# Performance work log

Measured on AMD Instinct MI355X. Metric: run time of the kernel, lower is better.

Reference implementation:

```python
import jax, jax.numpy as jnp
import numpy as np

N_NODES = 50000
N_EDGES = 600000
F_NODE = 128
F_EDGE = 32
MSG = 32


def setup_inputs() -> dict:
    key = jax.random.key(0)
    k1, k2, k3, k4, k5, k6, k7 = jax.random.split(key, 7)
    node_features = jax.random.normal(k1, (N_NODES, F_NODE), dtype=jnp.float32)
    edge_node_indices = jax.random.randint(k2, (2, N_EDGES), 0, N_NODES, dtype=jnp.int64)
    edge_features = jax.random.normal(k3, (N_EDGES, F_EDGE), dtype=jnp.float32)
    edge_in = 2 * F_NODE + F_EDGE  # 288
    node_in = F_NODE + MSG  # 160
    s_e = 1.0 / np.sqrt(edge_in)
    s_n = 1.0 / np.sqrt(node_in)
    We = jax.random.uniform(k4, (edge_in, MSG), dtype=jnp.float32, minval=-s_e, maxval=s_e)
    be = jax.random.uniform(k5, (MSG,), dtype=jnp.float32, minval=-s_e, maxval=s_e)
    Wn = jax.random.uniform(k6, (node_in, F_NODE), dtype=jnp.float32, minval=-s_n, maxval=s_n)
    bn = jax.random.uniform(k7, (F_NODE,), dtype=jnp.float32, minval=-s_n, maxval=s_n)
    return {
        "node_features": node_features,
        "edge_node_indices": edge_node_indices,
        "edge_features": edge_features,
        "We": We, "be": be, "Wn": Wn, "bn": bn,
    }


def reference(node_features, edge_node_indices, edge_features, We, be, Wn, bn):
    node0, node1 = edge_node_indices[0], edge_node_indices[1]
    # gather endpoint features per edge: [E, 2*Fn + Fe]
    msg_in = jnp.concatenate(
        [node_features[node0], node_features[node1], edge_features], axis=1
    )
    messages = jax.nn.relu(msg_in @ We + be)  # [E, MSG]
    # scatter-sum messages into source nodes (scatter index = node0)
    msg_sums = jax.ops.segment_sum(messages, node0, num_segments=node_features.shape[0])
    node_in = jnp.concatenate([node_features, msg_sums], axis=1)  # [N, Fn+MSG]
    return jax.nn.relu(node_in @ Wn + bn)  # [N, Fn]
```

## Files before the change

### kernel.cpp

```cpp
#include <hip/hip_runtime.h>

#define N_NODES 50000
#define N_EDGES 600000
#define F_NODE 128
#define F_EDGE 32
#define MSG 32
#define NPB 32
#define CHK 128
#define QB64 ((N_NODES + 63) / 64)
#define FBLOCKS ((N_NODES + NPB - 1) / NPB)
#define CBLOCKS ((N_EDGES + 255) / 256)

typedef float v2f __attribute__((ext_vector_type(2)));

__device__ __forceinline__ unsigned short f2bf(float f) {
    union { float f; unsigned int u; } v; v.f = f;
    unsigned int r = v.u + 0x7fffu + ((v.u >> 16) & 1u);
    return (unsigned short)(r >> 16);
}

#define BAR_LGKM() do {                                           \
    asm volatile("s_waitcnt lgkmcnt(0)" ::: "memory");            \
    __builtin_amdgcn_s_barrier();                                 \
    asm volatile("" ::: "memory");                                \
} while (0)

__global__ __launch_bounds__(256)
void hist_kernel(const float* __restrict__ nf,
                 const float* __restrict__ We,
                 const float* __restrict__ be,
                 const int* __restrict__ idx,
                 unsigned short* __restrict__ Q,
                 unsigned short* __restrict__ P0g,
                 int* __restrict__ deg,
                 int* __restrict__ rank)
{
    if (blockIdx.x >= QB64) {
        int e = (blockIdx.x - QB64) * 256 + threadIdx.x;
        if (e < N_EDGES) {
            int n = idx[e];
            if ((unsigned)n >= (unsigned)N_NODES) n = 0;
            rank[e] = atomicAdd(&deg[n], 1);
        }
        return;
    }
    __shared__ float sInT[32 * 64];
    __shared__ float sWeA[32 * 32];
    __shared__ float sWeB[32 * 32];

    const int tid = threadIdx.x;
    const int n0b = blockIdx.x * 64;
    const int ng = tid & 31;
    const int og = tid >> 5;

    v2f accA[4], accB[4];
#pragma unroll
    for (int j = 0; j < 4; ++j) { accA[j] = (v2f){0.f, 0.f}; accB[j] = (v2f){0.f, 0.f}; }

    for (int kc = 0; kc < 4; ++kc) {
        __syncthreads();
        ((float4*)sWeA)[tid] = ((const float4*)(We + kc * 32 * MSG))[tid];
        ((float4*)sWeB)[tid] = ((const float4*)(We + (128 + kc * 32) * MSG))[tid];
        {
            int nl = tid >> 2, q = tid & 3;
            int n = n0b + nl; if (n >= N_NODES) n = N_NODES - 1;
            const float4* src4 = (const float4*)(nf + (size_t)n * F_NODE + kc * 32);
#pragma unroll
            for (int h = 0; h < 2; ++h) {
                float4 v = src4[q * 2 + h];
                int kl = q * 8 + h * 4;
                sInT[(kl + 0) * 64 + nl] = v.x;
                sInT[(kl + 1) * 64 + nl] = v.y;
                sInT[(kl + 2) * 64 + nl] = v.z;
                sInT[(kl + 3) * 64 + nl] = v.w;
            }
        }
        __syncthreads();
#pragma unroll
        for (int k = 0; k < 32; ++k) {
            v2f m = *(const v2f*)&sInT[k * 64 + 2 * ng];
            float4 wa = *(const float4*)&sWeA[k * 32 + og * 4];
            float4 wb = *(const float4*)&sWeB[k * 32 + og * 4];
            accA[0] += m * wa.x; accA[1] += m * wa.y;
            accA[2] += m * wa.z; accA[3] += m * wa.w;
            accB[0] += m * wb.x; accB[1] += m * wb.y;
            accB[2] += m * wb.z; accB[3] += m * wb.w;
        }
    }
    float bloc[4];
#pragma unroll
    for (int j = 0; j < 4; ++j) bloc[j] = be[og * 4 + j];
#pragma unroll
    for (int i = 0; i < 2; ++i) {
        int n = n0b + 2 * ng + i;
        if (n < N_NODES) {
            ushort4 oq, op;
            oq.x = f2bf(accB[0][i]); oq.y = f2bf(accB[1][i]);
            oq.z = f2bf(accB[2][i]); oq.w = f2bf(accB[3][i]);
            op.x = f2bf(accA[0][i] + bloc[0]); op.y = f2bf(accA[1][i] + bloc[1]);
            op.z = f2bf(accA[2][i] + bloc[2]); op.w = f2bf(accA[3][i] + bloc[3]);
            *(ushort4*)(Q   + (size_t)n * MSG + og * 4) = oq;
            *(ushort4*)(P0g + (size_t)n * MSG + og * 4) = op;
        }
    }
}

__global__ __launch_bounds__(1024)
void scan_kernel(int* __restrict__ deg_cursor) {
    __shared__ int wsum[16];
    __shared__ int wpre[16];
    const int t = threadIdx.x;
    const int lane = t & 63;
    const int wid = t >> 6;
    const int N4 = N_NODES / 4;
    const int NT = (N4 + 1023) / 1024;
    int run = 0;
    int4 vnext = make_int4(0, 0, 0, 0);
    if (t < N4) vnext = ((const int4*)deg_cursor)[t];
    for (int tt = 0; tt < NT; ++tt) {
        int4 v = vnext;
        if (tt + 1 < NT) {
            int ni = (tt + 1) * 1024 + t;
            vnext = (ni < N4) ? ((const int4*)deg_cursor)[ni] : make_int4(0, 0, 0, 0);
        }
        int s = v.x + v.y + v.z + v.w;
        int x = s;
#pragma unroll
        for (int d = 1; d < 64; d <<= 1) {
            int u = __shfl_up(x, (unsigned)d, 64);
            if (lane >= d) x += u;
        }
        if (lane == 63) wsum[wid] = x;
        BAR_LGKM();
        if (wid == 0) {
            int ss = (lane < 16) ? wsum[lane] : 0;
#pragma unroll
            for (int d = 1; d < 16; d <<= 1) {
                int u = __shfl_up(ss, (unsigned)d, 64);
                if (lane >= d) ss += u;
            }
            if (lane < 16) wpre[lane] = ss;
        }
        BAR_LGKM();
        int wexcl = (wid > 0) ? wpre[wid - 1] : 0;
        int total = wpre[15];
        int i4 = tt * 1024 + t;
        if (i4 < N4) {
            int base = run + wexcl + (x - s);
            int4 o;
            o.x = base;
            o.y = base + v.x;
            o.z = base + v.x + v.y;
            o.w = base + v.x + v.y + v.z;
            ((int4*)deg_cursor)[i4] = o;
        }
        run += total;
        BAR_LGKM();
    }
}

__global__ void place_kernel(const int* __restrict__ idx,
                             const int* __restrict__ startArr,
                             const int* __restrict__ rank,
                             int* __restrict__ perm) {
    int e = blockIdx.x * 256 + threadIdx.x;
    if (e < N_EDGES) {
        int n = idx[e];
        if ((unsigned)n >= (unsigned)N_NODES) n = 0;
        int p = startArr[n] + rank[e];
        if ((unsigned)p < (unsigned)N_EDGES) perm[p] = e;
    }
}

__global__ __launch_bounds__(256, 4)
void fused_kernel(const float* __restrict__ nf,
                  const int* __restrict__ idx,
                  const float* __restrict__ ef,
                  const float* __restrict__ We,
                  const float* __restrict__ Wn,
                  const float* __restrict__ bn,
                  const int* __restrict__ perm,
                  const int* __restrict__ startArr,
                  const unsigned short* __restrict__ Q,
                  const unsigned short* __restrict__ P0g,
                  float* __restrict__ out)
{
    __shared__ __align__(16) float S[9892];
    float* sBuf = S;
    float* sMsg = S + 4096;
    float* sWeC = S + 8192;
    unsigned short* sP0h = (unsigned short*)(S + 9216);
    int* sNL  = (int*)(S + 9728);
    int* sOff = (int*)(S + 9856);
    float* sWn   = S;
    float* sInT2 = S + 4096;

    const int tid = threadIdx.x;
    const int n0b = blockIdx.x * NPB;

    if (tid <= NPB) {
        int nn = n0b + tid;
        int v = (nn < N_NODES) ? startArr[nn] : N_EDGES;
        if (v < 0) v = 0;
        if (v > N_EDGES) v = N_EDGES;
        sOff[tid] = v;
    }
    ((float4*)sWeC)[tid] = ((const float4*)(We + 256 * MSG))[tid];
    if (tid < 128) {
        int r = tid >> 2, c = (tid & 3) * 8;
        int n = n0b + r; if (n >= N_NODES) n = N_NODES - 1;
        *(uint4*)(sP0h + r * MSG + c) = *(const uint4*)(P0g + (size_t)n * MSG + c);
    }
    __syncthreads();

    const int rs = sOff[0];
    const int re = sOff[NPB];

    float msum[4];
#pragma unroll
    for (int j = 0; j < 4; ++j) msum[j] = 0.f;
    const int rnl = tid >> 3;
    const int rq4 = (tid & 7) * 4;
    const int gx  = (rq4 >> 3) << 2;

    const int eq = tid & 31;
    const int cq = tid >> 5;
    const int g1 = (cq >> 1) & 3;
    const int el = tid >> 1;
    const int h2 = tid & 1;

    int n1r = 0;
    int pe_next = 0, pe_next2 = 0;
    float4 efr[4];
#pragma unroll
    for (int q = 0; q < 4; ++q) efr[q] = make_float4(0.f, 0.f, 0.f, 0.f);

    if (rs < re) {
        int e0 = rs + el;
        int pe0 = 0;
        if (e0 < re) {
            pe0 = perm[e0];
            if ((unsigned)pe0 >= (unsigned)N_EDGES) pe0 = 0;
            if (h2 == 0) {
                int tn = idx[N_EDGES + pe0];
                if ((unsigned)tn >= (unsigned)N_NODES) tn = 0;
                n1r = tn;
            }
        }
        const float4* ef4 = (const float4*)(ef + (size_t)pe0 * F_EDGE + h2 * 16);
#pragma unroll
        for (int q = 0; q < 4; ++q) efr[q] = ef4[q];
        int e1 = rs + CHK + el;
        if (e1 < re) {
            int p = perm[e1];
            if ((unsigned)p >= (unsigned)N_EDGES) p = 0;
            pe_next = p;
        }
        pe_next2 = pe_next;
    }

    for (int cs = rs; cs < re; cs += CHK) {
        pe_next = pe_next2;
        {
#pragma unroll
            for (int q = 0; q < 4; ++q) {
                float4 v = efr[q];
                int g = (h2 * 2 + (q >> 1)) & 3;
                int ctw = ((el & ~3) ^ (g << 2)) + (el & 3);
                int r0 = (h2 * 16 + q * 4) * CHK;
                sBuf[r0 + 0 * CHK + ctw] = v.x;
                sBuf[r0 + 1 * CHK + ctw] = v.y;
                sBuf[r0 + 2 * CHK + ctw] = v.z;
                sBuf[r0 + 3 * CHK + ctw] = v.w;
            }
            if (h2 == 0) {
                int e = cs + el;
                int ln = 0;
                if (e < re) {
                    int lo = 0, hi = NPB;
#pragma unroll
                    for (int s = 0; s < 5; ++s) {
                        int mid = (lo + hi) >> 1;
                        if (sOff[mid] <= e) lo = mid; else hi = mid;
                    }
                    ln = lo;
                }
                sNL[el] = (ln << 20) | n1r;
            }
            int e1 = cs + CHK + el;
            if (e1 < re) {
                int pe1 = pe_next;
                if (h2 == 0) {
                    int tn = idx[N_EDGES + pe1];
                    if ((unsigned)tn >= (unsigned)N_NODES) tn = 0;
                    n1r = tn;
                }
                const float4* ef4 = (const float4*)(ef + (size_t)pe1 * F_EDGE + h2 * 16);
#pragma unroll
                for (int q = 0; q < 4; ++q) efr[q] = ef4[q];
            } else if (h2 == 0) n1r = 0;
            int e2 = cs + 2 * CHK + el;
            if (e2 < re) {
                int p = perm[e2];
                if ((unsigned)p >= (unsigned)N_EDGES) p = 0;
                pe_next2 = p;
            } else pe_next2 = 0;
        }
        BAR_LGKM();

        int4 nlq = *(const int4*)&sNL[4 * eq];
        int nlv[4] = { nlq.x, nlq.y, nlq.z, nlq.w };
        uint2 qv[4];
#pragma unroll
        for (int i = 0; i < 4; ++i)
            qv[i] = *(const uint2*)(Q + (size_t)(nlv[i] & 0xFFFFF) * MSG + cq * 4);

        v2f accp[4][2];
#pragma unroll
        for (int j = 0; j < 4; ++j) { accp[j][0] = (v2f){0.f,0.f}; accp[j][1] = (v2f){0.f,0.f}; }

#pragma unroll
        for (int k = 0; k < 32; ++k) {
            float4 m4 = *(const float4*)&sBuf[k * CHK + ((4 * eq) ^ (((k >> 3) & 3) << 2))];
            float4 w  = *(const float4*)&sWeC[k * 32 + cq * 4];
            v2f m01 = (v2f){m4.x, m4.y}, m23 = (v2f){m4.z, m4.w};
            accp[0][0] += m01 * w.x; accp[0][1] += m23 * w.x;
            accp[1][0] += m01 * w.y; accp[1][1] += m23 * w.y;
            accp[2][0] += m01 * w.z; accp[2][1] += m23 * w.z;
            accp[3][0] += m01 * w.w; accp[3][1] += m23 * w.w;
        }

        {
            uint2 pv[4];
#pragma unroll
            for (int i = 0; i < 4; ++i)
                pv[i] = *(const uint2*)(sP0h + (nlv[i] >> 20) * MSG + cq * 4);
            int sb = (4 * eq) ^ (g1 << 2);
#pragma unroll
            for (int j = 0; j < 4; ++j) {
                float sv[4];
#pragma unroll
                for (int i = 0; i < 4; ++i) {
                    unsigned qu = (j < 2) ? qv[i].x : qv[i].y;
                    unsigned pu = (j < 2) ? pv[i].x : pv[i].y;
                    float qf = __uint_as_float((j & 1) ? (qu & 0xffff0000u) : (qu << 16));
                    float pf = __uint_as_float((j & 1) ? (pu & 0xffff0000u) : (pu << 16));
                    sv[i] = fmaxf(accp[j][i >> 1][i & 1] + pf + qf, 0.f);
                }
                *(float4*)&sMsg[(cq * 4 + j) * CHK + sb] =
                    make_float4(sv[0], sv[1], sv[2], sv[3]);
            }
        }
        BAR_LGKM();

        {
            int lo = sOff[rnl] - cs;     if (lo < 0) lo = 0;
            int hi = sOff[rnl + 1] - cs; if (hi > CHK) hi = CHK;
            for (int elr = lo; elr < hi; ++elr) {
                int ebase = ((elr & ~3) ^ gx) + (elr & 3);
#pragma unroll
                for (int j = 0; j < 4; ++j)
                    msum[j] += sMsg[(rq4 + j) * CHK + ebase];
            }
        }
    }

    const int png = tid & 7;
    const int pcg = tid >> 3;

    v2f acc2[4][2];
#pragma unroll
    for (int j = 0; j < 4; ++j) { acc2[j][0] = (v2f){0.f,0.f}; acc2[j][1] = (v2f){0.f,0.f}; }

    for (int kc = 0; kc < 5; ++kc) {
        __syncthreads();
        {
            const float4* w4 = (const float4*)(Wn + (size_t)kc * 32 * 128);
            float4* s4 = (float4*)sWn;
#pragma unroll
            for (int i = 0; i < 4; ++i) s4[tid + 256 * i] = w4[tid + 256 * i];
        }
        {
            if (kc < 4) {
                int nl = tid >> 3, q = tid & 7;
                int n = n0b + nl; if (n >= N_NODES) n = N_NODES - 1;
                float4 v = *(const float4*)(nf + (size_t)n * F_NODE + kc * 32 + q * 4);
#pragma unroll
                for (int h = 0; h < 4; ++h) {
                    int r = q * 4 + h;
                    sInT2[r * 32 + (nl ^ ((r & 7) << 2))] = (&v.x)[h];
                }
            } else {
#pragma unroll
                for (int h = 0; h < 4; ++h) {
                    int r = rq4 + h;
                    sInT2[r * 32 + (rnl ^ ((r & 7) << 2))] = msum[h];
                }
            }
        }
        __syncthreads();

#pragma unroll
        for (int k = 0; k < 32; ++k) {
            float4 m4 = *(const float4*)&sInT2[k * 32 + ((4 * png) ^ ((k & 7) << 2))];
            float4 w  = *(const float4*)&sWn[k * 128 + 4 * pcg];
            v2f m01 = (v2f){m4.x, m4.y}, m23 = (v2f){m4.z, m4.w};
            acc2[0][0] += m01 * w.x; acc2[0][1] += m23 * w.x;
            acc2[1][0] += m01 * w.y; acc2[1][1] += m23 * w.y;
            acc2[2][0] += m01 * w.z; acc2[2][1] += m23 * w.z;
            acc2[3][0] += m01 * w.w; acc2[3][1] += m23 * w.w;
        }
    }

    {
        float4 bnv = *(const float4*)(bn + 4 * pcg);
#pragma unroll
        for (int p = 0; p < 2; ++p)
#pragma unroll
            for (int l = 0; l < 2; ++l) {
                int n = n0b + 4 * png + 2 * p + l;
                if (n < N_NODES) {
                    float4 v;
                    v.x = fmaxf(acc2[0][p][l] + bnv.x, 0.f);
                    v.y = fmaxf(acc2[1][p][l] + bnv.y, 0.f);
                    v.z = fmaxf(acc2[2][p][l] + bnv.z, 0.f);
                    v.w = fmaxf(acc2[3][p][l] + bnv.w, 0.f);
                    *(float4*)(out + (size_t)n * F_NODE + 4 * pcg) = v;
                }
            }
    }
}

extern "C" void kernel_launch(void* const* d_in, const int* in_sizes, int n_in,
                              void* d_out, int out_size, void* d_ws, size_t ws_size,
                              hipStream_t stream) {
    const float* nf  = (const float*)d_in[0];
    const int*   idx = (const int*)d_in[1];
    const float* ef  = (const float*)d_in[2];
    const float* We  = (const float*)d_in[3];
    const float* be  = (const float*)d_in[4];
    const float* Wn  = (const float*)d_in[5];
    const float* bn  = (const float*)d_in[6];
    float* out = (float*)d_out;

    int* deg  = (int*)d_ws;
    int* rank = deg + N_NODES;
    int* perm = rank + N_EDGES;
    unsigned short* Q   = (unsigned short*)(perm + N_EDGES);
    unsigned short* P0g = Q + (size_t)N_NODES * MSG;

    hipMemsetAsync(deg, 0, (size_t)N_NODES * sizeof(int), stream);

    hist_kernel<<<QB64 + CBLOCKS, 256, 0, stream>>>(nf, We, be, idx, Q, P0g, deg, rank);
    scan_kernel<<<1, 1024, 0, stream>>>(deg);
    place_kernel<<<CBLOCKS, 256, 0, stream>>>(idx, deg, rank, perm);

    fused_kernel<<<FBLOCKS, 256, 0, stream>>>(
        nf, idx, ef, We, Wn, bn, perm, deg, Q, P0g, out);
}
```

Baseline: 260.3 us.

## Precompute node-feature half of node MLP in histogram kernel as bf16

Moves the node_features@Wn[0:128] + bn part of the node update out of the fused kernel and into extra blocks of the histogram kernel. Those blocks write the partial product to a bf16 workspace buffer, so the fused kernel only does the message-sum chunk (K=32) and adds the stored partial. This is meant to shorten the fused kernel's tail and overlap the dense GEMM with the edge histogram work. In exchange it adds a 50000x128 bf16 write and read, and rounding the partial to bf16 reduces accuracy.

After: 655.3 us. 152% more time.

```diff
diff --git a/kernel.cpp b/kernel.cpp
--- a/kernel.cpp
+++ b/kernel.cpp
@@ -29,14 +29,20 @@
 void hist_kernel(const float* __restrict__ nf,
                  const float* __restrict__ We,
                  const float* __restrict__ be,
+                 const float* __restrict__ Wn,
+                 const float* __restrict__ bn,
                  const int* __restrict__ idx,
                  unsigned short* __restrict__ Q,
                  unsigned short* __restrict__ P0g,
+                 unsigned short* __restrict__ OP,
                  int* __restrict__ deg,
                  int* __restrict__ rank)
 {
-    if (blockIdx.x >= QB64) {
-        int e = (blockIdx.x - QB64) * 256 + threadIdx.x;
+    __shared__ __align__(16) float S[6144];
+    const int tid = threadIdx.x;
+
+    if (blockIdx.x >= 2 * QB64) {
+        int e = (blockIdx.x - 2 * QB64) * 256 + tid;
         if (e < N_EDGES) {
             int n = idx[e];
             if ((unsigned)n >= (unsigned)N_NODES) n = 0;
@@ -44,63 +50,138 @@
         }
         return;
     }
-    __shared__ float sInT[32 * 64];
-    __shared__ float sWeA[32 * 32];
-    __shared__ float sWeB[32 * 32];
-
-    const int tid = threadIdx.x;
-    const int n0b = blockIdx.x * 64;
-    const int ng = tid & 31;
-    const int og = tid >> 5;
-
-    v2f accA[4], accB[4];
-#pragma unroll
-    for (int j = 0; j < 4; ++j) { accA[j] = (v2f){0.f, 0.f}; accB[j] = (v2f){0.f, 0.f}; }
-
-    for (int kc = 0; kc < 4; ++kc) {
-        __syncthreads();
-        ((float4*)sWeA)[tid] = ((const float4*)(We + kc * 32 * MSG))[tid];
-        ((float4*)sWeB)[tid] = ((const float4*)(We + (128 + kc * 32) * MSG))[tid];
-        {
-            int nl = tid >> 2, q = tid & 3;
-            int n = n0b + nl; if (n >= N_NODES) n = N_NODES - 1;
-            const float4* src4 = (const float4*)(nf + (size_t)n * F_NODE + kc * 32);
-#pragma unroll
-            for (int h = 0; h < 2; ++h) {
-                float4 v = src4[q * 2 + h];
-                int kl = q * 8 + h * 4;
-                sInT[(kl + 0) * 64 + nl] = v.x;
-                sInT[(kl + 1) * 64 + nl] = v.y;
-                sInT[(kl + 2) * 64 + nl] = v.z;
-                sInT[(kl + 3) * 64 + nl] = v.w;
-            }
-        }
-        __syncthreads();
-#pragma unroll
-        for (int k = 0; k < 32; ++k) {
-            v2f m = *(const v2f*)&sInT[k * 64 + 2 * ng];
-            float4 wa = *(const float4*)&sWeA[k * 32 + og * 4];
-            float4 wb = *(const float4*)&sWeB[k * 32 + og * 4];
-            accA[0] += m * wa.x; accA[1] += m * wa.y;
-            accA[2] += m * wa.z; accA[3] += m * wa.w;
-            accB[0] += m * wb.x; accB[1] += m * wb.y;
-            accB[2] += m * wb.z; accB[3] += m * wb.w;
-        }
-    }
-    float bloc[4];
-#pragma unroll
-    for (int j = 0; j < 4; ++j) bloc[j] = be[og * 4 + j];
-#pragma unroll
-    for (int i = 0; i < 2; ++i) {
-        int n = n0b + 2 * ng + i;
-        if (n < N_NODES) {
-            ushort4 oq, op;
-            oq.x = f2bf(accB[0][i]); oq.y = f2bf(accB[1][i]);
-            oq.z = f2bf(accB[2][i]); oq.w = f2bf(accB[3][i]);
-            op.x = f2bf(accA[0][i] + bloc[0]); op.y = f2bf(accA[1][i] + bloc[1]);
-            op.z = f2bf(accA[2][i] + bloc[2]); op.w = f2bf(accA[3][i] + bloc[3]);
-            *(ushort4*)(Q   + (size_t)n * MSG + og * 4) = oq;
-            *(ushort4*)(P0g + (size_t)n * MSG + og * 4) = op;
+
+    if (blockIdx.x >= QB64) {
+        float* sInT = S;
+        float* sWn  = S + 2048;
+        const int n0b = (blockIdx.x - QB64) * 64;
+        const int png2 = tid >> 4;
+        const int pcg2 = tid & 15;
+
+        v2f accC[8][2];
+#pragma unroll
+        for (int j = 0; j < 8; ++j) { accC[j][0] = (v2f){0.f,0.f}; accC[j][1] = (v2f){0.f,0.f}; }
+
+        for (int kc = 0; kc < 4; ++kc) {
+            __syncthreads();
+            {
+                const float4* w4 = (const float4*)(Wn + (size_t)kc * 32 * 128);
+                float4* s4 = (float4*)sWn;
+#pragma unroll
+                for (int i = 0; i < 4; ++i) s4[tid + 256 * i] = w4[tid + 256 * i];
+            }
+            {
+                int nl = tid >> 2, q = tid & 3;
+                int n = n0b + nl; if (n >= N_NODES) n = N_NODES - 1;
+                const float4* src4 = (const float4*)(nf + (size_t)n * F_NODE + kc * 32);
+#pragma unroll
+                for (int h = 0; h < 2; ++h) {
+                    float4 v = src4[q * 2 + h];
+                    int kl = q * 8 + h * 4;
+                    sInT[(kl + 0) * 64 + nl] = v.x;
+                    sInT[(kl + 1) * 64 + nl] = v.y;
+                    sInT[(kl + 2) * 64 + nl] = v.z;
+                    sInT[(kl + 3) * 64 + nl] = v.w;
+                }
+            }
+            __syncthreads();
+#pragma unroll
+            for (int k = 0; k < 32; ++k) {
+                float4 m4 = *(const float4*)&sInT[k * 64 + 4 * png2];
+                float4 w0 = *(const float4*)&sWn[k * 128 + 4 * pcg2];
+                float4 w1 = *(const float4*)&sWn[k * 128 + 64 + 4 * pcg2];
+                v2f m01 = (v2f){m4.x, m4.y}, m23 = (v2f){m4.z, m4.w};
+                accC[0][0] += m01 * w0.x; accC[0][1] += m23 * w0.x;
+                accC[1][0] += m01 * w0.y; accC[1][1] += m23 * w0.y;
+                accC[2][0] += m01 * w0.z; accC[2][1] += m23 * w0.z;
+                accC[3][0] += m01 * w0.w; accC[3][1] += m23 * w0.w;
+                accC[4][0] += m01 * w1.x; accC[4][1] += m23 * w1.x;
+                accC[5][0] += m01 * w1.y; accC[5][1] += m23 * w1.y;
+                accC[6][0] += m01 * w1.z; accC[6][1] += m23 * w1.z;
+                accC[7][0] += m01 * w1.w; accC[7][1] += m23 * w1.w;
+            }
+        }
+        float4 b0 = *(const float4*)(bn + 4 * pcg2);
+        float4 b1 = *(const float4*)(bn + 64 + 4 * pcg2);
+#pragma unroll
+        for (int p = 0; p < 2; ++p)
+#pragma unroll
+            for (int l = 0; l < 2; ++l) {
+                int n = n0b + 4 * png2 + 2 * p + l;
+                if (n < N_NODES) {
+                    ushort4 o0, o1;
+                    o0.x = f2bf(accC[0][p][l] + b0.x);
+                    o0.y = f2bf(accC[1][p][l] + b0.y);
+                    o0.z = f2bf(accC[2][p][l] + b0.z);
+                    o0.w = f2bf(accC[3][p][l] + b0.w);
+                    o1.x = f2bf(accC[4][p][l] + b1.x);
+                    o1.y = f2bf(accC[5][p][l] + b1.y);
+                    o1.z = f2bf(accC[6][p][l] + b1.z);
+                    o1.w = f2bf(accC[7][p][l] + b1.w);
+                    *(ushort4*)(OP + (size_t)n * F_NODE + 4 * pcg2) = o0;
+                    *(ushort4*)(OP + (size_t)n * F_NODE + 64 + 4 * pcg2) = o1;
+                }
+            }
+        return;
+    }
+
+    {
+        float* sInT = S;
+        float* sWeA = S + 2048;
+        float* sWeB = S + 3072;
+        const int n0b = blockIdx.x * 64;
+        const int ng = tid & 31;
+        const int og = tid >> 5;
+
+        v2f accA[4], accB[4];
+#pragma unroll
+        for (int j = 0; j < 4; ++j) { accA[j] = (v2f){0.f, 0.f}; accB[j] = (v2f){0.f, 0.f}; }
+
+        for (int kc = 0; kc < 4; ++kc) {
+            __syncthreads();
+            ((float4*)sWeA)[tid] = ((const float4*)(We + kc * 32 * MSG))[tid];
+            ((float4*)sWeB)[tid] = ((const float4*)(We + (128 + kc * 32) * MSG))[tid];
+            {
+                int nl = tid >> 2, q = tid & 3;
+                int n = n0b + nl; if (n >= N_NODES) n = N_NODES - 1;
+                const float4* src4 = (const float4*)(nf + (size_t)n * F_NODE + kc * 32);
+#pragma unroll
+                for (int h = 0; h < 2; ++h) {
+                    float4 v = src4[q * 2 + h];
+                    int kl = q * 8 + h * 4;
+                    sInT[(kl + 0) * 64 + nl] = v.x;
+                    sInT[(kl + 1) * 64 + nl] = v.y;
+                    sInT[(kl + 2) * 64 + nl] = v.z;
+                    sInT[(kl + 3) * 64 + nl] = v.w;
+                }
+            }
+            __syncthreads();
+#pragma unroll
+            for (int k = 0; k < 32; ++k) {
+                v2f m = *(const v2f*)&sInT[k * 64 + 2 * ng];
+                float4 wa = *(const float4*)&sWeA[k * 32 + og * 4];
+                float4 wb = *(const float4*)&sWeB[k * 32 + og * 4];
+                accA[0] += m * wa.x; accA[1] += m * wa.y;
+                accA[2] += m * wa.z; accA[3] += m * wa.w;
+                accB[0] += m * wb.x; accB[1] += m * wb.y;
+                accB[2] += m * wb.z; accB[3] += m * wb.w;
+            }
+        }
+        float bloc[4];
+#pragma unroll
+        for (int j = 0; j < 4; ++j) bloc[j] = be[og * 4 + j];
+#pragma unroll
+        for (int i = 0; i < 2; ++i) {
+            int n = n0b + 2 * ng + i;
+            if (n < N_NODES) {
+                ushort4 oq, op;
+                oq.x = f2bf(accB[0][i]); oq.y = f2bf(accB[1][i]);
+                oq.z = f2bf(accB[2][i]); oq.w = f2bf(accB[3][i]);
+                op.x = f2bf(accA[0][i] + bloc[0]); op.y = f2bf(accA[1][i] + bloc[1]);
+                op.z = f2bf(accA[2][i] + bloc[2]); op.w = f2bf(accA[3][i] + bloc[3]);
+                *(ushort4*)(Q   + (size_t)n * MSG + og * 4) = oq;
+                *(ushort4*)(P0g + (size_t)n * MSG + og * 4) = op;
+            }
         }
     }
 }
@@ -178,11 +259,11 @@
                   const float* __restrict__ ef,
                   const float* __restrict__ We,
                   const float* __restrict__ Wn,
-                  const float* __restrict__ bn,
                   const int* __restrict__ perm,
                   const int* __restrict__ startArr,
                   const unsigned short* __restrict__ Q,
                   const unsigned short* __restrict__ P0g,
+                  const unsigned short* __restrict__ OP,
                   float* __restrict__ out)
 {
     __shared__ __align__(16) float S[9892];
@@ -192,7 +273,7 @@
     unsigned short* sP0h = (unsigned short*)(S + 9216);
     int* sNL  = (int*)(S + 9728);
     int* sOff = (int*)(S + 9856);
-    float* sWn   = S;
+    float* sWn2  = S;
     float* sInT2 = S + 4096;
 
     const int tid = threadIdx.x;
@@ -368,63 +449,48 @@
     const int png = tid & 7;
     const int pcg = tid >> 3;
 
+    __syncthreads();
+    {
+        const float4* w4 = (const float4*)(Wn + (size_t)128 * 128);
+        float4* s4 = (float4*)sWn2;
+#pragma unroll
+        for (int i = 0; i < 4; ++i) s4[tid + 256 * i] = w4[tid + 256 * i];
+#pragma unroll
+        for (int h = 0; h < 4; ++h) {
+            int r = rq4 + h;
+            sInT2[r * 32 + (rnl ^ ((r & 7) << 2))] = msum[h];
+        }
+    }
+    __syncthreads();
+
     v2f acc2[4][2];
 #pragma unroll
     for (int j = 0; j < 4; ++j) { acc2[j][0] = (v2f){0.f,0.f}; acc2[j][1] = (v2f){0.f,0.f}; }
 
-    for (int kc = 0; kc < 5; ++kc) {
-        __syncthreads();
-        {
-            const float4* w4 = (const float4*)(Wn + (size_t)kc * 32 * 128);
-            float4* s4 = (float4*)sWn;
-#pragma unroll
-            for (int i = 0; i < 4; ++i) s4[tid + 256 * i] = w4[tid + 256 * i];
-        }
-        {
-            if (kc < 4) {
-                int nl = tid >> 3, q = tid & 7;
-                int n = n0b + nl; if (n >= N_NODES) n = N_NODES - 1;
-                float4 v = *(const float4*)(nf + (size_t)n * F_NODE + kc * 32 + q * 4);
-#pragma unroll
-                for (int h = 0; h < 4; ++h) {
-                    int r = q * 4 + h;
-                    sInT2[r * 32 + (nl ^ ((r & 7) << 2))] = (&v.x)[h];
-                }
-            } else {
-#pragma unroll
-                for (int h = 0; h < 4; ++h) {
-                    int r = rq4 + h;
-                    sInT2[r * 32 + (rnl ^ ((r & 7) << 2))] = msum[h];
-                }
-            }
-        }
-        __syncthreads();
-
-#pragma unroll
-        for (int k = 0; k < 32; ++k) {
-            float4 m4 = *(const float4*)&sInT2[k * 32 + ((4 * png) ^ ((k & 7) << 2))];
-            float4 w  = *(const float4*)&sWn[k * 128 + 4 * pcg];
-            v2f m01 = (v2f){m4.x, m4.y}, m23 = (v2f){m4.z, m4.w};
-            acc2[0][0] += m01 * w.x; acc2[0][1] += m23 * w.x;
-            acc2[1][0] += m01 * w.y; acc2[1][1] += m23 * w.y;
-            acc2[2][0] += m01 * w.z; acc2[2][1] += m23 * w.z;
-            acc2[3][0] += m01 * w.w; acc2[3][1] += m23 * w.w;
-        }
+#pragma unroll
+    for (int k = 0; k < 32; ++k) {
+        float4 m4 = *(const float4*)&sInT2[k * 32 + ((4 * png) ^ ((k & 7) << 2))];
+        float4 w  = *(const float4*)&sWn2[k * 128 + 4 * pcg];
+        v2f m01 = (v2f){m4.x, m4.y}, m23 = (v2f){m4.z, m4.w};
+        acc2[0][0] += m01 * w.x; acc2[0][1] += m23 * w.x;
+        acc2[1][0] += m01 * w.y; acc2[1][1] += m23 * w.y;
+        acc2[2][0] += m01 * w.z; acc2[2][1] += m23 * w.z;
+        acc2[3][0] += m01 * w.w; acc2[3][1] += m23 * w.w;
     }
 
     {
-        float4 bnv = *(const float4*)(bn + 4 * pcg);
 #pragma unroll
         for (int p = 0; p < 2; ++p)
 #pragma unroll
             for (int l = 0; l < 2; ++l) {
                 int n = n0b + 4 * png + 2 * p + l;
                 if (n < N_NODES) {
+                    ushort4 po = *(const ushort4*)(OP + (size_t)n * F_NODE + 4 * pcg);
                     float4 v;
-                    v.x = fmaxf(acc2[0][p][l] + bnv.x, 0.f);
-                    v.y = fmaxf(acc2[1][p][l] + bnv.y, 0.f);
-                    v.z = fmaxf(acc2[2][p][l] + bnv.z, 0.f);
-                    v.w = fmaxf(acc2[3][p][l] + bnv.w, 0.f);
+                    v.x = fmaxf(acc2[0][p][l] + __uint_as_float((unsigned)po.x << 16), 0.f);
+                    v.y = fmaxf(acc2[1][p][l] + __uint_as_float((unsigned)po.y << 16), 0.f);
+                    v.z = fmaxf(acc2[2][p][l] + __uint_as_float((unsigned)po.z << 16), 0.f);
+                    v.w = fmaxf(acc2[3][p][l] + __uint_as_float((unsigned)po.w << 16), 0.f);
                     *(float4*)(out + (size_t)n * F_NODE + 4 * pcg) = v;
                 }
             }
@@ -448,13 +514,15 @@
     int* perm = rank + N_EDGES;
     unsigned short* Q   = (unsigned short*)(perm + N_EDGES);
     unsigned short* P0g = Q + (size_t)N_NODES * MSG;
+    unsigned short* OP  = P0g + (size_t)N_NODES * MSG;
 
     hipMemsetAsync(deg, 0, (size_t)N_NODES * sizeof(int), stream);
 
-    hist_kernel<<<QB64 + CBLOCKS, 256, 0, stream>>>(nf, We, be, idx, Q, P0g, deg, rank);
+    hist_kernel<<<2 * QB64 + CBLOCKS, 256, 0, stream>>>(
+        nf, We, be, Wn, bn, idx, Q, P0g, OP, deg, rank);
     scan_kernel<<<1, 1024, 0, stream>>>(deg);
     place_kernel<<<CBLOCKS, 256, 0, stream>>>(idx, deg, rank, perm);
 
     fused_kernel<<<FBLOCKS, 256, 0, stream>>>(
-        nf, idx, ef, We, Wn, bn, perm, deg, Q, P0g, out);
+        nf, idx, ef, We, Wn, perm, deg, Q, P0g, OP, out);
 }
```
